# Performance work log

Measured on AMD Instinct MI355X. Metric: run time of the kernel, lower is better.

Reference implementation:

```python
import jax, jax.numpy as jnp
import numpy as np

DIM = 1024
HEADS = 16
HEAD_DIM = DIM // HEADS
HIDDEN = 4 * DIM
EPS = 1e-5

def _layernorm(x, w, b):
    mu = jnp.mean(x, axis=-1, keepdims=True)
    var = jnp.mean(jnp.square(x - mu), axis=-1, keepdims=True)
    return (x - mu) * jax.lax.rsqrt(var + EPS) * w + b

def setup_inputs() -> dict:
    key = jax.random.key(0)
    ks = jax.random.split(key, 8)
    B, N, C = 4, 1024, DIM
    s = lambda fan_in: 1.0 / np.sqrt(fan_in)
    return {
        "x": jax.random.normal(ks[0], (B, N, C), dtype=jnp.float32),
        "ln1_w": jnp.ones((C,), jnp.float32),
        "ln1_b": jnp.zeros((C,), jnp.float32),
        "qkv_w": jax.random.normal(ks[1], (3 * C, C), jnp.float32) * s(C),
        "proj_w": jax.random.normal(ks[2], (C, C), jnp.float32) * s(C),
        "proj_b": jnp.zeros((C,), jnp.float32),
        "ln2_w": jnp.ones((C,), jnp.float32),
        "ln2_b": jnp.zeros((C,), jnp.float32),
        "fc1_w": jax.random.normal(ks[3], (HIDDEN, C), jnp.float32) * s(C),
        "fc1_b": jnp.zeros((HIDDEN,), jnp.float32),
        "fc2_w": jax.random.normal(ks[4], (C, HIDDEN), jnp.float32) * s(HIDDEN),
        "fc2_b": jnp.zeros((C,), jnp.float32),
    }

def reference(x, ln1_w, ln1_b, qkv_w, proj_w, proj_b, ln2_w, ln2_b, fc1_w, fc1_b, fc2_w, fc2_b):
    B, N, C = x.shape
    H, D = HEADS, HEAD_DIM
    scale = D ** -0.5
    # --- attention branch (pre-norm) ---
    h = _layernorm(x, ln1_w, ln1_b)
    qkv = jnp.einsum('bnc,oc->bno', h, qkv_w)          # [B,N,3C], no bias (qkv_bias=False)
    qkv = qkv.reshape(B, N, 3, H, D)
    q = jnp.transpose(qkv[:, :, 0], (0, 2, 1, 3))       # [B,H,N,D]
    k = jnp.transpose(qkv[:, :, 1], (0, 2, 1, 3))
    v = jnp.transpose(qkv[:, :, 2], (0, 2, 1, 3))
    attn = jnp.einsum('bhnd,bhmd->bhnm', q, k) * scale  # [B,H,N,N]
    attn = jax.nn.softmax(attn, axis=-1)
    o = jnp.einsum('bhnm,bhmd->bhnd', attn, v)          # [B,H,N,D]
    o = jnp.transpose(o, (0, 2, 1, 3)).reshape(B, N, C)
    o = jnp.einsum('bnc,oc->bno', o, proj_w) + proj_b
    x = x + o
    # --- MLP branch (pre-norm); drop=0.0 -> identity ---
    h = _layernorm(x, ln2_w, ln2_b)
    h = jnp.einsum('bnc,hc->bnh', h, fc1_w) + fc1_b
    h = jax.nn.gelu(h, approximate=False)               # nn.GELU exact erf form
    h = jnp.einsum('bnh,ch->bnc', h, fc2_w) + fc2_b
    return x + h
```

## Files before the change

kernel.cpp:

```cpp
#include <hip/hip_runtime.h>
#include <hip/hip_bf16.h>
#include <math.h>
#include <stdint.h>

#define SEQ 1024
#define CDIM 1024
#define NHEAD 16
#define HIDDEN 4096
#define BATCH 4
#define MROWS (BATCH*SEQ)

using bf16x8 = __attribute__((ext_vector_type(8))) short;
using f32x4  = __attribute__((ext_vector_type(4))) float;

__device__ __forceinline__ short f2bf(float f) {
    union { float f; uint32_t u; } c; c.f = f;
    const uint32_t u = c.u + 0x7FFFu + ((c.u >> 16) & 1u);
    return (short)(u >> 16);
}

__device__ __forceinline__ float gelu_exact(float v) {
    return 0.5f * v * (1.0f + erff(v * 0.70710678118654752440f));
}

__device__ __forceinline__ void gload_lds16(const short* g, short* lds) {
    __builtin_amdgcn_global_load_lds(
        (const __attribute__((address_space(1))) void*)(uintptr_t)g,
        (__attribute__((address_space(3))) void*)(uintptr_t)lds,
        16, 0, 0);
}

__global__ void cvt_bf16_kernel(const float* __restrict__ in, short* __restrict__ out) {
    const size_t i = ((size_t)blockIdx.x * 256 + threadIdx.x) * 8;
    const float4 a = *(const float4*)(in + i);
    const float4 b = *(const float4*)(in + i + 4);
    bf16x8 s;
    s[0] = f2bf(a.x); s[1] = f2bf(a.y); s[2] = f2bf(a.z); s[3] = f2bf(a.w);
    s[4] = f2bf(b.x); s[5] = f2bf(b.y); s[6] = f2bf(b.z); s[7] = f2bf(b.w);
    *(bf16x8*)(out + i) = s;
}

__global__ void ln_kernel(const float* __restrict__ x, const float* __restrict__ w,
                          const float* __restrict__ b, short* __restrict__ out) {
    const int row = blockIdx.x;
    const int t = threadIdx.x;
    const float4* xr = (const float4*)(x + (size_t)row * CDIM);
    float4 v = xr[t];
    float s  = v.x + v.y + v.z + v.w;
    float sq = v.x*v.x + v.y*v.y + v.z*v.z + v.w*v.w;
    #pragma unroll
    for (int off = 32; off; off >>= 1) {
        s  += __shfl_down(s, off);
        sq += __shfl_down(sq, off);
    }
    __shared__ float ss[4], ssq[4];
    const int wid = t >> 6, lane = t & 63;
    if (lane == 0) { ss[wid] = s; ssq[wid] = sq; }
    __syncthreads();
    s  = ss[0] + ss[1] + ss[2] + ss[3];
    sq = ssq[0] + ssq[1] + ssq[2] + ssq[3];
    const float mu  = s * (1.0f / CDIM);
    const float var = sq * (1.0f / CDIM) - mu * mu;
    const float rs  = rsqrtf(var + 1e-5f);
    const float4 wv = ((const float4*)w)[t];
    const float4 bv = ((const float4*)b)[t];
    short4 o;
    o.x = f2bf((v.x - mu) * rs * wv.x + bv.x);
    o.y = f2bf((v.y - mu) * rs * wv.y + bv.y);
    o.z = f2bf((v.z - mu) * rs * wv.z + bv.z);
    o.w = f2bf((v.w - mu) * rs * wv.w + bv.w);
    *(short4*)(out + (size_t)row * CDIM + t * 4) = o;
}

template<bool BIAS, bool RES, bool GELU_, bool OUTBF16>
__global__ __launch_bounds__(512) void gemm8p(
    const short* __restrict__ A, const short* __restrict__ B,
    const float* __restrict__ bias, const float* __restrict__ res,
    void* __restrict__ Cv, int M, int N, int K)
{
    __shared__ __align__(16) short As[2][256 * 64];
    __shared__ __align__(16) short Bs[2][256 * 64];
    const int t = threadIdx.x;
    const int w = t >> 6, l = t & 63;
    const int wm = w >> 2, wn = w & 3;

    const int lid = blockIdx.y * gridDim.x + blockIdx.x;
    const int xcd = lid & 7, c = lid >> 3;
    const int by = (xcd >> 1) * 4 + (c >> 3);
    const int bx = (xcd & 1) * 8 + (c & 7);
    const int m0 = by * 256, n0 = bx * 256;

    const int trow = t >> 3;
    const int k8s = ((t & 7) ^ (trow & 7)) * 8;
    const short* Ag = A + (size_t)(m0 + trow) * K + k8s;
    const short* Bg = B + (size_t)(n0 + trow) * K + k8s;

    const int fr = l & 15, g = l >> 4;
    const int sw = fr & 7;
    const int ak0 = (g ^ sw) * 8;
    const int ak1 = ((4 + g) ^ sw) * 8;
    int aoff[8], boff[4];
    #pragma unroll
    for (int mf = 0; mf < 8; ++mf) aoff[mf] = (wm * 128 + mf * 16 + fr) * 64;
    #pragma unroll
    for (int nf = 0; nf < 4; ++nf) boff[nf] = (wn * 64 + nf * 16 + fr) * 64;

    f32x4 acc[8][4] = {};

#define STAGE8(Gb, LDSb, kt, h)                                             \
    {                                                                       \
        gload_lds16((Gb) + (size_t)((h) * 128) * K + (kt) * 64,             \
                    (LDSb) + ((h) * 128 + w * 8) * 64);                     \
        gload_lds16((Gb) + (size_t)((h) * 128 + 64) * K + (kt) * 64,        \
                    (LDSb) + ((h) * 128 + 64 + w * 8) * 64);                \
    }

    STAGE8(Ag, As[0], 0, 0); STAGE8(Ag, As[0], 0, 1);
    STAGE8(Bg, Bs[0], 0, 0); STAGE8(Bg, Bs[0], 0, 1);
    asm volatile("s_waitcnt vmcnt(0)" ::: "memory");
    __builtin_amdgcn_s_barrier();

    const int T = K / 64;
    for (int kt = 0; kt < T; ++kt) {
        short* curA = &As[kt & 1][0];
        short* curB = &Bs[kt & 1][0];
        short* nxtA = &As[(kt & 1) ^ 1][0];
        short* nxtB = &Bs[(kt & 1) ^ 1][0];
        const bool pre = (kt + 1 < T);
        bf16x8 bfr[4], af[4];

        if (pre) STAGE8(Ag, nxtA, kt + 1, 0);
        #pragma unroll
        for (int nf = 0; nf < 4; ++nf) bfr[nf] = *(const bf16x8*)&curB[boff[nf] + ak0];
        #pragma unroll
        for (int mf = 0; mf < 4; ++mf) af[mf] = *(const bf16x8*)&curA[aoff[mf] + ak0];
        __builtin_amdgcn_s_barrier();
        __builtin_amdgcn_s_setprio(1);
        #pragma unroll
        for (int mf = 0; mf < 4; ++mf)
            #pragma unroll
            for (int nf = 0; nf < 4; ++nf)
                acc[mf][nf] = __builtin_amdgcn_mfma_f32_16x16x32_bf16(af[mf], bfr[nf], acc[mf][nf], 0, 0, 0);
        __builtin_amdgcn_s_setprio(0);
        __builtin_amdgcn_s_barrier();

        if (pre) STAGE8(Ag, nxtA, kt + 1, 1);
        #pragma unroll
        for (int mf = 0; mf < 4; ++mf) af[mf] = *(const bf16x8*)&curA[aoff[4 + mf] + ak0];
        __builtin_amdgcn_s_barrier();
        __builtin_amdgcn_s_setprio(1);
        #pragma unroll
        for (int mf = 0; mf < 4; ++mf)
            #pragma unroll
            for (int nf = 0; nf < 4; ++nf)
                acc[4 + mf][nf] = __builtin_amdgcn_mfma_f32_16x16x32_bf16(af[mf], bfr[nf], acc[4 + mf][nf], 0, 0, 0);
        __builtin_amdgcn_s_setprio(0);
        __builtin_amdgcn_s_barrier();

        if (pre) STAGE8(Bg, nxtB, kt + 1, 0);
        #pragma unroll
        for (int nf = 0; nf < 4; ++nf) bfr[nf] = *(const bf16x8*)&curB[boff[nf] + ak1];
        #pragma unroll
        for (int mf = 0; mf < 4; ++mf) af[mf] = *(const bf16x8*)&curA[aoff[mf] + ak1];
        __builtin_amdgcn_s_barrier();
        __builtin_amdgcn_s_setprio(1);
        #pragma unroll
        for (int mf = 0; mf < 4; ++mf)
            #pragma unroll
            for (int nf = 0; nf < 4; ++nf)
                acc[mf][nf] = __builtin_amdgcn_mfma_f32_16x16x32_bf16(af[mf], bfr[nf], acc[mf][nf], 0, 0, 0);
        __builtin_amdgcn_s_setprio(0);
        __builtin_amdgcn_s_barrier();

        if (pre) STAGE8(Bg, nxtB, kt + 1, 1);
        #pragma unroll
        for (int mf = 0; mf < 4; ++mf) af[mf] = *(const bf16x8*)&curA[aoff[4 + mf] + ak1];
        __builtin_amdgcn_s_barrier();
        __builtin_amdgcn_s_setprio(1);
        #pragma unroll
        for (int mf = 0; mf < 4; ++mf)
            #pragma unroll
            for (int nf = 0; nf < 4; ++nf)
                acc[4 + mf][nf] = __builtin_amdgcn_mfma_f32_16x16x32_bf16(af[mf], bfr[nf], acc[4 + mf][nf], 0, 0, 0);
        __builtin_amdgcn_s_setprio(0);
        asm volatile("s_waitcnt vmcnt(0)" ::: "memory");
        __builtin_amdgcn_s_barrier();
    }
#undef STAGE8

    const int lr4 = (l >> 4) * 4, lc = l & 15;
    #pragma unroll
    for (int mf = 0; mf < 8; ++mf) {
        #pragma unroll
        for (int nf = 0; nf < 4; ++nf) {
            const int col = n0 + wn * 64 + nf * 16 + lc;
            const float bv = BIAS ? bias[col] : 0.0f;
            #pragma unroll
            for (int r = 0; r < 4; ++r) {
                const int row = m0 + wm * 128 + mf * 16 + lr4 + r;
                float v = acc[mf][nf][r] + bv;
                if (GELU_) v = gelu_exact(v);
                if (RES)   v += res[(size_t)row * N + col];
                if (OUTBF16) ((short*)Cv)[(size_t)row * N + col] = f2bf(v);
                else         ((float*)Cv)[(size_t)row * N + col] = v;
            }
        }
    }
}

__global__ __launch_bounds__(512) void qkv8p(
    const short* __restrict__ A, const short* __restrict__ B,
    short* __restrict__ qkvb, short* __restrict__ VT, int K)
{
    __shared__ __align__(16) short As[2][256 * 64];
    __shared__ __align__(16) short Bs[2][256 * 64];
    const int t = threadIdx.x;
    const int w = t >> 6, l = t & 63;
    const int wm = w >> 2, wn = w & 3;

    const int lid = blockIdx.y * gridDim.x + blockIdx.x;
    const int swz = (lid & 7) * 24 + (lid >> 3);
    const int bx = swz % 12, by = swz / 12;
    const int m0 = by * 256, n0 = bx * 256;

    const int trow = t >> 3;
    const int k8s = ((t & 7) ^ (trow & 7)) * 8;
    const short* Ag = A + (size_t)(m0 + trow) * K + k8s;
    const short* Bg = B + (size_t)(n0 + trow) * K + k8s;

    const int fr = l & 15, g = l >> 4;
    const int sw = fr & 7;
    const int ak0 = (g ^ sw) * 8;
    const int ak1 = ((4 + g) ^ sw) * 8;
    int aoff[8], boff[4];
    #pragma unroll
    for (int mf = 0; mf < 8; ++mf) aoff[mf] = (wm * 128 + mf * 16 + fr) * 64;
    #pragma unroll
    for (int nf = 0; nf < 4; ++nf) boff[nf] = (wn * 64 + nf * 16 + fr) * 64;

    f32x4 acc[8][4] = {};

#define STAGE8(Gb, LDSb, kt, h)                                             \
    {                                                                       \
        gload_lds16((Gb) + (size_t)((h) * 128) * K + (kt) * 64,             \
                    (LDSb) + ((h) * 128 + w * 8) * 64);                     \
        gload_lds16((Gb) + (size_t)((h) * 128 + 64) * K + (kt) * 64,        \
                    (LDSb) + ((h) * 128 + 64 + w * 8) * 64);                \
    }

    STAGE8(Ag, As[0], 0, 0); STAGE8(Ag, As[0], 0, 1);
    STAGE8(Bg, Bs[0], 0, 0); STAGE8(Bg, Bs[0], 0, 1);
    asm volatile("s_waitcnt vmcnt(0)" ::: "memory");
    __builtin_amdgcn_s_barrier();

    const int T = K / 64;
    for (int kt = 0; kt < T; ++kt) {
        short* curA = &As[kt & 1][0];
        short* curB = &Bs[kt & 1][0];
        short* nxtA = &As[(kt & 1) ^ 1][0];
        short* nxtB = &Bs[(kt & 1) ^ 1][0];
        const bool pre = (kt + 1 < T);
        bf16x8 bfr[4], af[4];

        if (pre) STAGE8(Ag, nxtA, kt + 1, 0);
        #pragma unroll
        for (int nf = 0; nf < 4; ++nf) bfr[nf] = *(const bf16x8*)&curB[boff[nf] + ak0];
        #pragma unroll
        for (int mf = 0; mf < 4; ++mf) af[mf] = *(const bf16x8*)&curA[aoff[mf] + ak0];
        __builtin_amdgcn_s_barrier();
        __builtin_amdgcn_s_setprio(1);
        #pragma unroll
        for (int mf = 0; mf < 4; ++mf)
            #pragma unroll
            for (int nf = 0; nf < 4; ++nf)
                acc[mf][nf] = __builtin_amdgcn_mfma_f32_16x16x32_bf16(af[mf], bfr[nf], acc[mf][nf], 0, 0, 0);
        __builtin_amdgcn_s_setprio(0);
        __builtin_amdgcn_s_barrier();

        if (pre) STAGE8(Ag, nxtA, kt + 1, 1);
        #pragma unroll
        for (int mf = 0; mf < 4; ++mf) af[mf] = *(const bf16x8*)&curA[aoff[4 + mf] + ak0];
        __builtin_amdgcn_s_barrier();
        __builtin_amdgcn_s_setprio(1);
        #pragma unroll
        for (int mf = 0; mf < 4; ++mf)
            #pragma unroll
            for (int nf = 0; nf < 4; ++nf)
                acc[4 + mf][nf] = __builtin_amdgcn_mfma_f32_16x16x32_bf16(af[mf], bfr[nf], acc[4 + mf][nf], 0, 0, 0);
        __builtin_amdgcn_s_setprio(0);
        __builtin_amdgcn_s_barrier();

        if (pre) STAGE8(Bg, nxtB, kt + 1, 0);
        #pragma unroll
        for (int nf = 0; nf < 4; ++nf) bfr[nf] = *(const bf16x8*)&curB[boff[nf] + ak1];
        #pragma unroll
        for (int mf = 0; mf < 4; ++mf) af[mf] = *(const bf16x8*)&curA[aoff[mf] + ak1];
        __builtin_amdgcn_s_barrier();
        __builtin_amdgcn_s_setprio(1);
        #pragma unroll
        for (int mf = 0; mf < 4; ++mf)
            #pragma unroll
            for (int nf = 0; nf < 4; ++nf)
                acc[mf][nf] = __builtin_amdgcn_mfma_f32_16x16x32_bf16(af[mf], bfr[nf], acc[mf][nf], 0, 0, 0);
        __builtin_amdgcn_s_setprio(0);
        __builtin_amdgcn_s_barrier();

        if (pre) STAGE8(Bg, nxtB, kt + 1, 1);
        #pragma unroll
        for (int mf = 0; mf < 4; ++mf) af[mf] = *(const bf16x8*)&curA[aoff[4 + mf] + ak1];
        __builtin_amdgcn_s_barrier();
        __builtin_amdgcn_s_setprio(1);
        #pragma unroll
        for (int mf = 0; mf < 4; ++mf)
            #pragma unroll
            for (int nf = 0; nf < 4; ++nf)
                acc[4 + mf][nf] = __builtin_amdgcn_mfma_f32_16x16x32_bf16(af[mf], bfr[nf], acc[4 + mf][nf], 0, 0, 0);
        __builtin_amdgcn_s_setprio(0);
        asm volatile("s_waitcnt vmcnt(0)" ::: "memory");
        __builtin_amdgcn_s_barrier();
    }
#undef STAGE8

    const int lr4 = (l >> 4) * 4, lc = l & 15;
    if (n0 < 2048) {
        const float sc = (n0 < 1024) ? 0.125f : 1.0f;
        #pragma unroll
        for (int mf = 0; mf < 8; ++mf) {
            #pragma unroll
            for (int nf = 0; nf < 4; ++nf) {
                const int col = n0 + wn * 64 + nf * 16 + lc;
                #pragma unroll
                for (int r = 0; r < 4; ++r) {
                    const int row = m0 + wm * 128 + mf * 16 + lr4 + r;
                    qkvb[(size_t)row * 2048 + col] = f2bf(acc[mf][nf][r] * sc);
                }
            }
        }
    } else {
        #pragma unroll
        for (int mf = 0; mf < 8; ++mf) {
            const int row0 = m0 + wm * 128 + mf * 16 + lr4;
            const int b = row0 >> 10, nseq = row0 & 1023;
            #pragma unroll
            for (int nf = 0; nf < 4; ++nf) {
                const int c2 = n0 - 2048 + wn * 64 + nf * 16 + lc;
                const int h = c2 >> 6, d = c2 & 63;
                short4 v4;
                v4.x = f2bf(acc[mf][nf][0]); v4.y = f2bf(acc[mf][nf][1]);
                v4.z = f2bf(acc[mf][nf][2]); v4.w = f2bf(acc[mf][nf][3]);
                *(short4*)&VT[(((size_t)(b * 16 + h) * 64 + d) * 1024) + nseq] = v4;
            }
        }
    }
}

template<int BN, bool BIAS, bool RES, bool GELU_, bool OUTBF16>
__global__ __launch_bounds__(256) void mgemm(
    const short* __restrict__ A, const short* __restrict__ B,
    const float* __restrict__ bias, const float* __restrict__ res,
    void* __restrict__ Cv, int M, int N, int K)
{
    constexpr int MF = (BN == 128) ? 4 : 2;
    __shared__ __align__(16) short As[3][128 * 32];
    __shared__ __align__(16) short Bs[3][BN * 32];
    const int t = threadIdx.x;
    const int w = t >> 6, l = t & 63;

    const int gx = gridDim.x;
    const int nwg = gx * gridDim.y;
    const int lid = blockIdx.y * gx + blockIdx.x;
    const int swzb = (lid & 7) * (nwg >> 3) + (lid >> 3);
    const int bx = swzb % gx, by = swzb / gx;
    const int m0 = by * 128, n0 = bx * BN;

    const int wrow = (BN == 128) ? (w >> 1) * 64 : w * 32;
    const int wcol = (BN == 128) ? (w & 1) * 64 : 0;

    const int sk8 = ((l & 3) ^ ((l >> 3) & 3)) * 8;
    const short* agp0 = A + (size_t)(m0 + w * 32 + (l >> 2)) * K + sk8;
    const short* agp1 = agp0 + (size_t)16 * K;
    const short* bgp0;
    const short* bgp1 = nullptr;
    if (BN == 128) {
        bgp0 = B + (size_t)(n0 + w * 32 + (l >> 2)) * K + sk8;
        bgp1 = bgp0 + (size_t)16 * K;
    } else {
        bgp0 = B + (size_t)(n0 + w * 16 + (l >> 2)) * K + sk8;
    }

    const int fr = l & 15;
    const int rsw = (fr >> 1) & 3;
    int aoff[MF], boff[4];
    #pragma unroll
    for (int m = 0; m < MF; ++m) aoff[m] = (wrow + m * 16 + fr) * 32 + ((l >> 4) ^ rsw) * 8;
    #pragma unroll
    for (int n = 0; n < 4; ++n)  boff[n] = (wcol + n * 16 + fr) * 32 + ((l >> 4) ^ rsw) * 8;

    auto stage = [&](int k0, int buf) {
        short* ldsA = &As[buf][w * 1024];
        gload_lds16(agp0 + k0, ldsA);
        gload_lds16(agp1 + k0, ldsA + 512);
        if (BN == 128) {
            short* ldsB = &Bs[buf][w * 1024];
            gload_lds16(bgp0 + k0, ldsB);
            gload_lds16(bgp1 + k0, ldsB + 512);
        } else {
            gload_lds16(bgp0 + k0, &Bs[buf][w * 512]);
        }
    };

    f32x4 acc[MF][4] = {};
    const int T = K / 32;
    stage(0, 0);
    stage(32, 1);
    int cur = 0;
    for (int kt = 0; kt < T; ++kt) {
        if (kt < T - 1) {
            if constexpr (BN == 128) asm volatile("s_waitcnt vmcnt(4)" ::: "memory");
            else                     asm volatile("s_waitcnt vmcnt(3)" ::: "memory");
        } else {
            asm volatile("s_waitcnt vmcnt(0)" ::: "memory");
        }
        __builtin_amdgcn_sched_barrier(0);
        __builtin_amdgcn_s_barrier();
        __builtin_amdgcn_sched_barrier(0);
        if (kt + 2 < T) {
            int nb = kt + 2; nb -= (nb >= 3) ? ((nb / 3) * 3) : 0;
            stage((kt + 2) * 32, nb);
        }
        bf16x8 af[MF], bfr[4];
        #pragma unroll
        for (int m = 0; m < MF; ++m) af[m]  = *(const bf16x8*)&As[cur][aoff[m]];
        #pragma unroll
        for (int n = 0; n < 4; ++n)  bfr[n] = *(const bf16x8*)&Bs[cur][boff[n]];
        #pragma unroll
        for (int m = 0; m < MF; ++m)
            #pragma unroll
            for (int n = 0; n < 4; ++n)
                acc[m][n] = __builtin_amdgcn_mfma_f32_16x16x32_bf16(af[m], bfr[n], acc[m][n], 0, 0, 0);
        cur = (cur == 2) ? 0 : cur + 1;
    }

    const int lr4 = (l >> 4) * 4, lc = l & 15;
    #pragma unroll
    for (int m = 0; m < MF; ++m) {
        #pragma unroll
        for (int n = 0; n < 4; ++n) {
            const int col = n0 + wcol + n * 16 + lc;
            const float bv = BIAS ? bias[col] : 0.0f;
            #pragma unroll
            for (int r = 0; r < 4; ++r) {
                const int row = m0 + wrow + m * 16 + lr4 + r;
                float v = acc[m][n][r] + bv;
                if (GELU_) v = gelu_exact(v);
                if (RES)   v += res[(size_t)row * N + col];
                if (OUTBF16) ((short*)Cv)[(size_t)row * N + col] = f2bf(v);
                else         ((float*)Cv)[(size_t)row * N + col] = v;
            }
        }
    }
}

__global__ __launch_bounds__(256) void fattn(const short* __restrict__ qkvb,
                                             const short* __restrict__ VT,
                                             short* __restrict__ o) {
    const int lid = blockIdx.y * gridDim.x + blockIdx.x;
    const int bh = ((lid >> 7) << 3) | (lid & 7);
    const int q0 = ((lid >> 3) & 15) * 64;
    const int b = bh >> 4, h = bh & 15;
    const int t = threadIdx.x, w = t >> 6, l = t & 63;

    __shared__ __align__(16) short Ks[2][64 * 64];
    __shared__ __align__(16) short Vs[2][64 * 64];
    __shared__ __align__(16) short Ps[4][1024];

    const size_t qrow = (size_t)(b * SEQ + q0 + w * 16 + (l & 15)) * 2048 + h * 64;
    bf16x8 qf[2];
    qf[0] = *(const bf16x8*)&qkvb[qrow + (l >> 4) * 8];
    qf[1] = *(const bf16x8*)&qkvb[qrow + 32 + (l >> 4) * 8];

    const int srow = l >> 3;
    const int sc16 = (l & 7) ^ (srow & 7);
    const short* Kg = qkvb + 1024 + h * 64;
    const short* Vg = VT + (size_t)bh * 64 * 1024;

    f32x4 acc[4] = {};
    float mr = -1e30f, lr = 0.0f;
    const int q = l & 15;
    const int g4 = (l >> 4) & 3;

    auto stage = [&](int kt, int buf) {
        const int kv0 = kt * 64;
        #pragma unroll
        for (int i = 0; i < 2; ++i) {
            const int r0 = w * 16 + i * 8;
            gload_lds16(Kg + (size_t)(b * SEQ + kv0 + r0 + srow) * 2048 + sc16 * 8,
                        &Ks[buf][r0 * 64]);
            gload_lds16(Vg + (size_t)(r0 + srow) * 1024 + kv0 + sc16 * 8,
                        &Vs[buf][r0 * 64]);
        }
    };

    stage(0, 0);
    for (int kt = 0; kt < 16; ++kt) {
        const int cur = kt & 1;
        __syncthreads();
        if (kt + 1 < 16) stage(kt + 1, cur ^ 1);

        f32x4 sacc[4];
        #pragma unroll
        for (int nt = 0; nt < 4; ++nt) {
            f32x4 z = {};
            #pragma unroll
            for (int ks = 0; ks < 2; ++ks) {
                const int row = nt * 16 + (l & 15);
                const int c16 = (ks * 4 + (l >> 4)) ^ (row & 7);
                const bf16x8 kf = *(const bf16x8*)&Ks[cur][row * 64 + c16 * 8];
                z = __builtin_amdgcn_mfma_f32_16x16x32_bf16(kf, qf[ks], z, 0, 0, 0);
            }
            sacc[nt] = z;
        }
        float tm = sacc[0][0];
        #pragma unroll
        for (int nt = 0; nt < 4; ++nt)
            #pragma unroll
            for (int r = 0; r < 4; ++r) tm = fmaxf(tm, sacc[nt][r]);
        tm = fmaxf(tm, __shfl_xor(tm, 16));
        tm = fmaxf(tm, __shfl_xor(tm, 32));
        const bool norescale = __all(tm <= mr + 8.0f);
        float fac = 1.0f;
        if (!norescale) {
            const float nm = fmaxf(mr, tm);
            fac = __expf(mr - nm);
            mr = nm;
        }
        float p[4][4];
        float ts = 0.0f;
        #pragma unroll
        for (int nt = 0; nt < 4; ++nt)
            #pragma unroll
            for (int r = 0; r < 4; ++r) {
                p[nt][r] = __expf(sacc[nt][r] - mr);
                ts += p[nt][r];
            }
        ts += __shfl_xor(ts, 16);
        ts += __shfl_xor(ts, 32);
        lr = lr * fac + ts;
        if (!norescale) {
            float facv[4];
            #pragma unroll
            for (int r = 0; r < 4; ++r)
                facv[r] = __shfl(fac, (l & 48) + g4 * 4 + r);
            #pragma unroll
            for (int nt2 = 0; nt2 < 4; ++nt2)
                #pragma unroll
                for (int r = 0; r < 4; ++r)
                    acc[nt2][r] *= facv[r];
        }
        #pragma unroll
        for (int nt = 0; nt < 4; ++nt) {
            uint32_t lo, hi;
            asm("v_cvt_pk_bf16_f32 %0, %1, %2" : "=v"(lo) : "v"(p[nt][0]), "v"(p[nt][1]));
            asm("v_cvt_pk_bf16_f32 %0, %1, %2" : "=v"(hi) : "v"(p[nt][2]), "v"(p[nt][3]));
            const int kvb = nt * 16 + g4 * 4;
            const int addr = q * 64 + (((kvb >> 3) ^ (q & 7)) << 3) + (kvb & 7);
            *(uint2*)&Ps[w][addr] = make_uint2(lo, hi);
        }
        __builtin_amdgcn_s_waitcnt(0);
        #pragma unroll
        for (int ks = 0; ks < 2; ++ks) {
            const int ql = l & 15;
            const bf16x8 pa = *(const bf16x8*)&Ps[w][ql * 64 + ((ks * 32 + (l >> 4) * 8) ^ ((ql & 7) << 3))];
            #pragma unroll
            for (int nt2 = 0; nt2 < 4; ++nt2) {
                const int row = nt2 * 16 + (l & 15);
                const int c16 = (ks * 4 + (l >> 4)) ^ (row & 7);
                const bf16x8 vf = *(const bf16x8*)&Vs[cur][row * 64 + c16 * 8];
                acc[nt2] = __builtin_amdgcn_mfma_f32_16x16x32_bf16(pa, vf, acc[nt2], 0, 0, 0);
            }
        }
    }
    float rcpl = 1.0f / lr;
    #pragma unroll
    for (int r = 0; r < 4; ++r) {
        const float rcp = __shfl(rcpl, (l & 48) + g4 * 4 + r);
        const int qq = q0 + w * 16 + g4 * 4 + r;
        #pragma unroll
        for (int nt2 = 0; nt2 < 4; ++nt2) {
            const int d = nt2 * 16 + (l & 15);
            o[(size_t)(b * SEQ + qq) * CDIM + h * 64 + d] = f2bf(acc[nt2][r] * rcp);
        }
    }
}

extern "C" void kernel_launch(void* const* d_in, const int* in_sizes, int n_in,
                              void* d_out, int out_size, void* d_ws, size_t ws_size,
                              hipStream_t stream) {
    const float* x      = (const float*)d_in[0];
    const float* ln1_w  = (const float*)d_in[1];
    const float* ln1_b  = (const float*)d_in[2];
    const float* qkv_w  = (const float*)d_in[3];
    const float* proj_w = (const float*)d_in[4];
    const float* proj_b = (const float*)d_in[5];
    const float* ln2_w  = (const float*)d_in[6];
    const float* ln2_b  = (const float*)d_in[7];
    const float* fc1_w  = (const float*)d_in[8];
    const float* fc1_b  = (const float*)d_in[9];
    const float* fc2_w  = (const float*)d_in[10];
    const float* fc2_b  = (const float*)d_in[11];
    float* out = (float*)d_out;

    short* ws16  = (short*)d_ws;
    short* wqkv  = ws16;
    short* wproj = ws16 + 3145728;
    short* wfc1  = ws16 + 4194304;
    short* wfc2  = ws16 + 8388608;
    char*  wsb   = (char*)d_ws;
    short* qkvb  = (short*)(wsb + (size_t)24 * 1024 * 1024);
    short* VT    = (short*)(wsb + (size_t)40 * 1024 * 1024);
    short* mlp1  = (short*)(wsb + (size_t)24 * 1024 * 1024);
    short* hbuf  = (short*)(wsb + (size_t)72 * 1024 * 1024);

    cvt_bf16_kernel<<<1536, 256, 0, stream>>>(qkv_w, wqkv);
    cvt_bf16_kernel<<< 512, 256, 0, stream>>>(proj_w, wproj);
    cvt_bf16_kernel<<<2048, 256, 0, stream>>>(fc1_w, wfc1);
    cvt_bf16_kernel<<<2048, 256, 0, stream>>>(fc2_w, wfc2);

    ln_kernel<<<MROWS, 256, 0, stream>>>(x, ln1_w, ln1_b, hbuf);
    qkv8p<<<dim3(12, 16), 512, 0, stream>>>(hbuf, wqkv, qkvb, VT, 1024);
    fattn<<<dim3(16, 64), 256, 0, stream>>>(qkvb, VT, hbuf);
    mgemm<64,true,true,false,false><<<dim3(16, 32), 256, 0, stream>>>(
        hbuf, wproj, proj_b, x, out, MROWS, 1024, 1024);
    ln_kernel<<<MROWS, 256, 0, stream>>>(out, ln2_w, ln2_b, hbuf);
    gemm8p<true,false,true,true><<<dim3(16, 16), 512, 0, stream>>>(
        hbuf, wfc1, fc1_b, nullptr, mlp1, MROWS, 4096, 1024);
    mgemm<64,true,true,false,false><<<dim3(16, 32), 256, 0, stream>>>(
        mlp1, wfc2, fc2_b, out, out, MROWS, 1024, 4096);
}
```

Baseline: 230.0 us.

## Switch big GEMMs to three-stage BK=32 pipeline with single barrier per step

The 256x256 GEMM and QKV kernels move from double-buffered BK=64 tiles with four barriers per iteration to a three-buffer BK=32 ring. Loads are issued two steps ahead, and a partial vmcnt wait with one barrier gates each step. The LDS swizzle and load mapping are redone for the 32-wide rows, and the block swizzle is generalised to the grid size. The proj/fc2 GEMMs switch to a 128-wide tile template, and the attention kernel waits only on lgkmcnt. The aim is less barrier stalling and better latency hiding, at the cost of shorter K-steps and possible LDS bank conflicts.

```diff
diff --git a/kernel.cpp b/kernel.cpp
--- a/kernel.cpp
+++ b/kernel.cpp
@@ -73,68 +73,64 @@
 }
 
 template<bool BIAS, bool RES, bool GELU_, bool OUTBF16>
-__global__ __launch_bounds__(512) void gemm8p(
+__global__ __launch_bounds__(512) void gemm8k(
     const short* __restrict__ A, const short* __restrict__ B,
     const float* __restrict__ bias, const float* __restrict__ res,
     void* __restrict__ Cv, int M, int N, int K)
 {
-    __shared__ __align__(16) short As[2][256 * 64];
-    __shared__ __align__(16) short Bs[2][256 * 64];
+    __shared__ __align__(16) short As[3][256 * 32];
+    __shared__ __align__(16) short Bs[3][256 * 32];
     const int t = threadIdx.x;
     const int w = t >> 6, l = t & 63;
     const int wm = w >> 2, wn = w & 3;
 
-    const int lid = blockIdx.y * gridDim.x + blockIdx.x;
-    const int xcd = lid & 7, c = lid >> 3;
-    const int by = (xcd >> 1) * 4 + (c >> 3);
-    const int bx = (xcd & 1) * 8 + (c & 7);
+    const int gx = gridDim.x;
+    const int nwg = gx * gridDim.y;
+    const int lid = blockIdx.y * gx + blockIdx.x;
+    const int swz = (lid & 7) * (nwg >> 3) + (lid >> 3);
+    const int bx = swz % gx, by = swz / gx;
     const int m0 = by * 256, n0 = bx * 256;
 
-    const int trow = t >> 3;
-    const int k8s = ((t & 7) ^ (trow & 7)) * 8;
+    const int trow = w * 16 + (l >> 2);
+    const int k8s = ((l & 3) ^ ((l >> 3) & 3)) * 8;
     const short* Ag = A + (size_t)(m0 + trow) * K + k8s;
     const short* Bg = B + (size_t)(n0 + trow) * K + k8s;
 
     const int fr = l & 15, g = l >> 4;
-    const int sw = fr & 7;
-    const int ak0 = (g ^ sw) * 8;
-    const int ak1 = ((4 + g) ^ sw) * 8;
+    const int ak = (g ^ ((fr >> 1) & 3)) * 8;
     int aoff[8], boff[4];
     #pragma unroll
-    for (int mf = 0; mf < 8; ++mf) aoff[mf] = (wm * 128 + mf * 16 + fr) * 64;
-    #pragma unroll
-    for (int nf = 0; nf < 4; ++nf) boff[nf] = (wn * 64 + nf * 16 + fr) * 64;
+    for (int mf = 0; mf < 8; ++mf) aoff[mf] = (wm * 128 + mf * 16 + fr) * 32 + ak;
+    #pragma unroll
+    for (int nf = 0; nf < 4; ++nf) boff[nf] = (wn * 64 + nf * 16 + fr) * 32 + ak;
+
+    auto stage = [&](int kt, int buf) {
+        gload_lds16(Ag + (size_t)kt * 32,           &As[buf][w * 512]);
+        gload_lds16(Ag + (size_t)128 * K + kt * 32, &As[buf][128 * 32 + w * 512]);
+        gload_lds16(Bg + (size_t)kt * 32,           &Bs[buf][w * 512]);
+        gload_lds16(Bg + (size_t)128 * K + kt * 32, &Bs[buf][128 * 32 + w * 512]);
+    };
 
     f32x4 acc[8][4] = {};
-
-#define STAGE8(Gb, LDSb, kt, h)                                             \
-    {                                                                       \
-        gload_lds16((Gb) + (size_t)((h) * 128) * K + (kt) * 64,             \
-                    (LDSb) + ((h) * 128 + w * 8) * 64);                     \
-        gload_lds16((Gb) + (size_t)((h) * 128 + 64) * K + (kt) * 64,        \
-                    (LDSb) + ((h) * 128 + 64 + w * 8) * 64);                \
-    }
-
-    STAGE8(Ag, As[0], 0, 0); STAGE8(Ag, As[0], 0, 1);
-    STAGE8(Bg, Bs[0], 0, 0); STAGE8(Bg, Bs[0], 0, 1);
-    asm volatile("s_waitcnt vmcnt(0)" ::: "memory");
-    __builtin_amdgcn_s_barrier();
-
-    const int T = K / 64;
+    const int T = K / 32;
+    stage(0, 0);
+    stage(1, 1);
+    int cur = 0;
     for (int kt = 0; kt < T; ++kt) {
-        short* curA = &As[kt & 1][0];
-        short* curB = &Bs[kt & 1][0];
-        short* nxtA = &As[(kt & 1) ^ 1][0];
-        short* nxtB = &Bs[(kt & 1) ^ 1][0];
-        const bool pre = (kt + 1 < T);
+        if (kt < T - 1) asm volatile("s_waitcnt vmcnt(4)" ::: "memory");
+        else            asm volatile("s_waitcnt vmcnt(0)" ::: "memory");
+        __builtin_amdgcn_sched_barrier(0);
+        __builtin_amdgcn_s_barrier();
+        __builtin_amdgcn_sched_barrier(0);
+        if (kt + 2 < T) {
+            int nb = kt + 2; nb -= (nb >= 3) ? ((nb / 3) * 3) : 0;
+            stage(kt + 2, nb);
+        }
         bf16x8 bfr[4], af[4];
-
-        if (pre) STAGE8(Ag, nxtA, kt + 1, 0);
-        #pragma unroll
-        for (int nf = 0; nf < 4; ++nf) bfr[nf] = *(const bf16x8*)&curB[boff[nf] + ak0];
-        #pragma unroll
-        for (int mf = 0; mf < 4; ++mf) af[mf] = *(const bf16x8*)&curA[aoff[mf] + ak0];
-        __builtin_amdgcn_s_barrier();
+        #pragma unroll
+        for (int nf = 0; nf < 4; ++nf) bfr[nf] = *(const bf16x8*)&Bs[cur][boff[nf]];
+        #pragma unroll
+        for (int mf = 0; mf < 4; ++mf) af[mf] = *(const bf16x8*)&As[cur][aoff[mf]];
         __builtin_amdgcn_s_setprio(1);
         #pragma unroll
         for (int mf = 0; mf < 4; ++mf)
@@ -142,12 +138,8 @@
             for (int nf = 0; nf < 4; ++nf)
                 acc[mf][nf] = __builtin_amdgcn_mfma_f32_16x16x32_bf16(af[mf], bfr[nf], acc[mf][nf], 0, 0, 0);
         __builtin_amdgcn_s_setprio(0);
-        __builtin_amdgcn_s_barrier();
-
-        if (pre) STAGE8(Ag, nxtA, kt + 1, 1);
-        #pragma unroll
-        for (int mf = 0; mf < 4; ++mf) af[mf] = *(const bf16x8*)&curA[aoff[4 + mf] + ak0];
-        __builtin_amdgcn_s_barrier();
+        #pragma unroll
+        for (int mf = 0; mf < 4; ++mf) af[mf] = *(const bf16x8*)&As[cur][aoff[4 + mf]];
         __builtin_amdgcn_s_setprio(1);
         #pragma unroll
         for (int mf = 0; mf < 4; ++mf)
@@ -155,38 +147,8 @@
             for (int nf = 0; nf < 4; ++nf)
                 acc[4 + mf][nf] = __builtin_amdgcn_mfma_f32_16x16x32_bf16(af[mf], bfr[nf], acc[4 + mf][nf], 0, 0, 0);
         __builtin_amdgcn_s_setprio(0);
-        __builtin_amdgcn_s_barrier();
-
-        if (pre) STAGE8(Bg, nxtB, kt + 1, 0);
-        #pragma unroll
-        for (int nf = 0; nf < 4; ++nf) bfr[nf] = *(const bf16x8*)&curB[boff[nf] + ak1];
-        #pragma unroll
-        for (int mf = 0; mf < 4; ++mf) af[mf] = *(const bf16x8*)&curA[aoff[mf] + ak1];
-        __builtin_amdgcn_s_barrier();
-        __builtin_amdgcn_s_setprio(1);
-        #pragma unroll
-        for (int mf = 0; mf < 4; ++mf)
-            #pragma unroll
-            for (int nf = 0; nf < 4; ++nf)
-                acc[mf][nf] = __builtin_amdgcn_mfma_f32_16x16x32_bf16(af[mf], bfr[nf], acc[mf][nf], 0, 0, 0);
-        __builtin_amdgcn_s_setprio(0);
-        __builtin_amdgcn_s_barrier();
-
-        if (pre) STAGE8(Bg, nxtB, kt + 1, 1);
-        #pragma unroll
-        for (int mf = 0; mf < 4; ++mf) af[mf] = *(const bf16x8*)&curA[aoff[4 + mf] + ak1];
-        __builtin_amdgcn_s_barrier();
-        __builtin_amdgcn_s_setprio(1);
-        #pragma unroll
-        for (int mf = 0; mf < 4; ++mf)
-            #pragma unroll
-            for (int nf = 0; nf < 4; ++nf)
-                acc[4 + mf][nf] = __builtin_amdgcn_mfma_f32_16x16x32_bf16(af[mf], bfr[nf], acc[4 + mf][nf], 0, 0, 0);
-        __builtin_amdgcn_s_setprio(0);
-        asm volatile("s_waitcnt vmcnt(0)" ::: "memory");
-        __builtin_amdgcn_s_barrier();
-    }
-#undef STAGE8
+        cur = (cur == 2) ? 0 : cur + 1;
+    }
 
     const int lr4 = (l >> 4) * 4, lc = l & 15;
     #pragma unroll
@@ -208,66 +170,63 @@
     }
 }
 
-__global__ __launch_bounds__(512) void qkv8p(
+__global__ __launch_bounds__(512) void qkv8k(
     const short* __restrict__ A, const short* __restrict__ B,
     short* __restrict__ qkvb, short* __restrict__ VT, int K)
 {
-    __shared__ __align__(16) short As[2][256 * 64];
-    __shared__ __align__(16) short Bs[2][256 * 64];
+    __shared__ __align__(16) short As[3][256 * 32];
+    __shared__ __align__(16) short Bs[3][256 * 32];
     const int t = threadIdx.x;
     const int w = t >> 6, l = t & 63;
     const int wm = w >> 2, wn = w & 3;
 
-    const int lid = blockIdx.y * gridDim.x + blockIdx.x;
-    const int swz = (lid & 7) * 24 + (lid >> 3);
-    const int bx = swz % 12, by = swz / 12;
+    const int gx = gridDim.x;
+    const int nwg = gx * gridDim.y;
+    const int lid = blockIdx.y * gx + blockIdx.x;
+    const int swz = (lid & 7) * (nwg >> 3) + (lid >> 3);
+    const int bx = swz % gx, by = swz / gx;
     const int m0 = by * 256, n0 = bx * 256;
 
-    const int trow = t >> 3;
-    const int k8s = ((t & 7) ^ (trow & 7)) * 8;
+    const int trow = w * 16 + (l >> 2);
+    const int k8s = ((l & 3) ^ ((l >> 3) & 3)) * 8;
     const short* Ag = A + (size_t)(m0 + trow) * K + k8s;
     const short* Bg = B + (size_t)(n0 + trow) * K + k8s;
 
     const int fr = l & 15, g = l >> 4;
-    const int sw = fr & 7;
-    const int ak0 = (g ^ sw) * 8;
-    const int ak1 = ((4 + g) ^ sw) * 8;
+    const int ak = (g ^ ((fr >> 1) & 3)) * 8;
     int aoff[8], boff[4];
     #pragma unroll
-    for (int mf = 0; mf < 8; ++mf) aoff[mf] = (wm * 128 + mf * 16 + fr) * 64;
-    #pragma unroll
-    for (int nf = 0; nf < 4; ++nf) boff[nf] = (wn * 64 + nf * 16 + fr) * 64;
+    for (int mf = 0; mf < 8; ++mf) aoff[mf] = (wm * 128 + mf * 16 + fr) * 32 + ak;
+    #pragma unroll
+    for (int nf = 0; nf < 4; ++nf) boff[nf] = (wn * 64 + nf * 16 + fr) * 32 + ak;
+
+    auto stage = [&](int kt, int buf) {
+        gload_lds16(Ag + (size_t)kt * 32,           &As[buf][w * 512]);
+        gload_lds16(Ag + (size_t)128 * K + kt * 32, &As[buf][128 * 32 + w * 512]);
+        gload_lds16(Bg + (size_t)kt * 32,           &Bs[buf][w * 512]);
+        gload_lds16(Bg + (size_t)128 * K + kt * 32, &Bs[buf][128 * 32 + w * 512]);
+    };
 
     f32x4 acc[8][4] = {};
-
-#define STAGE8(Gb, LDSb, kt, h)                                             \
-    {                                                                       \
-        gload_lds16((Gb) + (size_t)((h) * 128) * K + (kt) * 64,             \
-                    (LDSb) + ((h) * 128 + w * 8) * 64);                     \
-        gload_lds16((Gb) + (size_t)((h) * 128 + 64) * K + (kt) * 64,        \
-                    (LDSb) + ((h) * 128 + 64 + w * 8) * 64);                \
-    }
-
-    STAGE8(Ag, As[0], 0, 0); STAGE8(Ag, As[0], 0, 1);
-    STAGE8(Bg, Bs[0], 0, 0); STAGE8(Bg, Bs[0], 0, 1);
-    asm volatile("s_waitcnt vmcnt(0)" ::: "memory");
-    __builtin_amdgcn_s_barrier();
-
-    const int T = K / 64;
+    const int T = K / 32;
+    stage(0, 0);
+    stage(1, 1);
+    int cur = 0;
     for (int kt = 0; kt < T; ++kt) {
-        short* curA = &As[kt & 1][0];
-        short* curB = &Bs[kt & 1][0];
-        short* nxtA = &As[(kt & 1) ^ 1][0];
-        short* nxtB = &Bs[(kt & 1) ^ 1][0];
-        const bool pre = (kt + 1 < T);
+        if (kt < T - 1) asm volatile("s_waitcnt vmcnt(4)" ::: "memory");
+        else            asm volatile("s_waitcnt vmcnt(0)" ::: "memory");
+        __builtin_amdgcn_sched_barrier(0);
+        __builtin_amdgcn_s_barrier();
+        __builtin_amdgcn_sched_barrier(0);
+        if (kt + 2 < T) {
+            int nb = kt + 2; nb -= (nb >= 3) ? ((nb / 3) * 3) : 0;
+            stage(kt + 2, nb);
+        }
         bf16x8 bfr[4], af[4];
-
-        if (pre) STAGE8(Ag, nxtA, kt + 1, 0);
-        #pragma unroll
-        for (int nf = 0; nf < 4; ++nf) bfr[nf] = *(const bf16x8*)&curB[boff[nf] + ak0];
-        #pragma unroll
-        for (int mf = 0; mf < 4; ++mf) af[mf] = *(const bf16x8*)&curA[aoff[mf] + ak0];
-        __builtin_amdgcn_s_barrier();
+        #pragma unroll
+        for (int nf = 0; nf < 4; ++nf) bfr[nf] = *(const bf16x8*)&Bs[cur][boff[nf]];
+        #pragma unroll
+        for (int mf = 0; mf < 4; ++mf) af[mf] = *(const bf16x8*)&As[cur][aoff[mf]];
         __builtin_amdgcn_s_setprio(1);
         #pragma unroll
         for (int mf = 0; mf < 4; ++mf)
@@ -275,12 +234,8 @@
             for (int nf = 0; nf < 4; ++nf)
                 acc[mf][nf] = __builtin_amdgcn_mfma_f32_16x16x32_bf16(af[mf], bfr[nf], acc[mf][nf], 0, 0, 0);
         __builtin_amdgcn_s_setprio(0);
-        __builtin_amdgcn_s_barrier();
-
-        if (pre) STAGE8(Ag, nxtA, kt + 1, 1);
-        #pragma unroll
-        for (int mf = 0; mf < 4; ++mf) af[mf] = *(const bf16x8*)&curA[aoff[4 + mf] + ak0];
-        __builtin_amdgcn_s_barrier();
+        #pragma unroll
+        for (int mf = 0; mf < 4; ++mf) af[mf] = *(const bf16x8*)&As[cur][aoff[4 + mf]];
         __builtin_amdgcn_s_setprio(1);
         #pragma unroll
         for (int mf = 0; mf < 4; ++mf)
@@ -288,38 +243,8 @@
             for (int nf = 0; nf < 4; ++nf)
                 acc[4 + mf][nf] = __builtin_amdgcn_mfma_f32_16x16x32_bf16(af[mf], bfr[nf], acc[4 + mf][nf], 0, 0, 0);
         __builtin_amdgcn_s_setprio(0);
-        __builtin_amdgcn_s_barrier();
-
-        if (pre) STAGE8(Bg, nxtB, kt + 1, 0);
-        #pragma unroll
-        for (int nf = 0; nf < 4; ++nf) bfr[nf] = *(const bf16x8*)&curB[boff[nf] + ak1];
-        #pragma unroll
-        for (int mf = 0; mf < 4; ++mf) af[mf] = *(const bf16x8*)&curA[aoff[mf] + ak1];
-        __builtin_amdgcn_s_barrier();
-        __builtin_amdgcn_s_setprio(1);
-        #pragma unroll
-        for (int mf = 0; mf < 4; ++mf)
-            #pragma unroll
-            for (int nf = 0; nf < 4; ++nf)
-                acc[mf][nf] = __builtin_amdgcn_mfma_f32_16x16x32_bf16(af[mf], bfr[nf], acc[mf][nf], 0, 0, 0);
-        __builtin_amdgcn_s_setprio(0);
-        __builtin_amdgcn_s_barrier();
-
-        if (pre) STAGE8(Bg, nxtB, kt + 1, 1);
-        #pragma unroll
-        for (int mf = 0; mf < 4; ++mf) af[mf] = *(const bf16x8*)&curA[aoff[4 + mf] + ak1];
-        __builtin_amdgcn_s_barrier();
-        __builtin_amdgcn_s_setprio(1);
-        #pragma unroll
-        for (int mf = 0; mf < 4; ++mf)
-            #pragma unroll
-            for (int nf = 0; nf < 4; ++nf)
-                acc[4 + mf][nf] = __builtin_amdgcn_mfma_f32_16x16x32_bf16(af[mf], bfr[nf], acc[4 + mf][nf], 0, 0, 0);
-        __builtin_amdgcn_s_setprio(0);
-        asm volatile("s_waitcnt vmcnt(0)" ::: "memory");
-        __builtin_amdgcn_s_barrier();
-    }
-#undef STAGE8
+        cur = (cur == 2) ? 0 : cur + 1;
+    }
 
     const int lr4 = (l >> 4) * 4, lc = l & 15;
     if (n0 < 2048) {
@@ -566,7 +491,7 @@
             const int addr = q * 64 + (((kvb >> 3) ^ (q & 7)) << 3) + (kvb & 7);
             *(uint2*)&Ps[w][addr] = make_uint2(lo, hi);
         }
-        __builtin_amdgcn_s_waitcnt(0);
+        asm volatile("s_waitcnt lgkmcnt(0)" ::: "memory");
         #pragma unroll
         for (int ks = 0; ks < 2; ++ks) {
             const int ql = l & 15;
@@ -627,13 +552,13 @@
     cvt_bf16_kernel<<<2048, 256, 0, stream>>>(fc2_w, wfc2);
 
     ln_kernel<<<MROWS, 256, 0, stream>>>(x, ln1_w, ln1_b, hbuf);
-    qkv8p<<<dim3(12, 16), 512, 0, stream>>>(hbuf, wqkv, qkvb, VT, 1024);
+    qkv8k<<<dim3(12, 16), 512, 0, stream>>>(hbuf, wqkv, qkvb, VT, 1024);
     fattn<<<dim3(16, 64), 256, 0, stream>>>(qkvb, VT, hbuf);
-    mgemm<64,true,true,false,false><<<dim3(16, 32), 256, 0, stream>>>(
+    mgemm<128,true,true,false,false><<<dim3(8, 32), 256, 0, stream>>>(
         hbuf, wproj, proj_b, x, out, MROWS, 1024, 1024);
     ln_kernel<<<MROWS, 256, 0, stream>>>(out, ln2_w, ln2_b, hbuf);
-    gemm8p<true,false,true,true><<<dim3(16, 16), 512, 0, stream>>>(
+    gemm8k<true,false,true,true><<<dim3(16, 16), 512, 0, stream>>>(
         hbuf, wfc1, fc1_b, nullptr, mlp1, MROWS, 4096, 1024);
-    mgemm<64,true,true,false,false><<<dim3(16, 32), 256, 0, stream>>>(
+    mgemm<128,true,true,false,false><<<dim3(8, 32), 256, 0, stream>>>(
         mlp1, wfc2, fc2_b, out, out, MROWS, 1024, 4096);
 }
```

Measured after the change: 225.5 us. -2.0%, faster.
